# Performance work log

Measured on AMD Instinct MI355X. Metric: run time of the kernel, lower is better.

The kernel has to match this reference:

```python
import jax, jax.numpy as jnp
import numpy as np

B, S, H, NH, HD = 2, 2048, 4096, 32, 128
NEG = jnp.finfo(jnp.float32).min


def rotate_half(x):
    x1, x2 = x[..., : x.shape[-1] // 2], x[..., x.shape[-1] // 2 :]
    return jnp.concatenate((-x2, x1), axis=-1)


def setup_inputs() -> dict:
    key = jax.random.key(0)
    ks = jax.random.split(key, 7)
    return {
        "hidden_states": jax.random.normal(ks[0], (B, S, H), jnp.float32),
        "cos": jax.random.uniform(ks[1], (1, 1, S, HD), jnp.float32),
        "sin": jax.random.uniform(ks[2], (1, 1, S, HD), jnp.float32),
        "Wq": jax.random.normal(ks[3], (H, H), jnp.float32) * 0.02,
        "Wk": jax.random.normal(ks[4], (HD, H), jnp.float32) * 0.02,
        "Wv": jax.random.normal(ks[5], (HD, H), jnp.float32) * 0.02,
        "Wd": jax.random.normal(ks[6], (H, H), jnp.float32) * 0.02,
    }


def reference(hidden_states, cos, sin, Wq, Wk, Wv, Wd):
    b, s, _ = hidden_states.shape
    q = (hidden_states @ Wq.T).reshape(b, s, NH, HD).transpose(0, 2, 1, 3)  # [B,NH,S,HD]
    k = (hidden_states @ Wk.T)[:, None, :, :]  # [B,1,S,HD] (multi-query)
    v = (hidden_states @ Wv.T)[:, None, :, :]
    # inline RoPE
    q = q * cos + rotate_half(q) * sin
    k = k * cos + rotate_half(k) * sin
    scale = 1.0 / jnp.sqrt(jnp.float32(HD))
    scores = jnp.einsum("bhqd,bhkd->bhqk", q, k) * scale
    # causal mask: additive finfo.min above diagonal
    causal = jnp.tril(jnp.ones((s, s), jnp.bool_))
    scores = scores + jnp.where(causal, 0.0, NEG)
    attn = jax.nn.softmax(scores, axis=-1)
    out = jnp.einsum("bhqk,bhkd->bhqd", attn, v)  # [B,NH,S,HD]
    out = out.transpose(0, 2, 1, 3).reshape(b, s, NH * HD)
    return out @ Wd.T
```

## Files before the change

kernel.cpp:

```cpp
#include <hip/hip_runtime.h>
#include <hip/hip_bf16.h>

constexpr int Bc  = 2;
constexpr int Sc  = 2048;
constexpr int Hc  = 4096;
constexpr int NHc = 32;
constexpr int HDc = 128;

typedef __attribute__((ext_vector_type(8))) __bf16 bf16x8;
typedef __attribute__((ext_vector_type(4))) __bf16 bf16x4;
typedef __attribute__((ext_vector_type(4))) float  f32x4;

#if defined(__has_builtin)
#if __has_builtin(__builtin_amdgcn_global_load_lds)
#define HAS_GLL 1
#endif
#endif
#ifndef HAS_GLL
#define HAS_GLL 0
#endif

__device__ __forceinline__ void gll16(const __bf16* g, __bf16* lds_base, int lane) {
#if HAS_GLL
    __builtin_amdgcn_global_load_lds((const __attribute__((address_space(1))) void*)g,
                                     (__attribute__((address_space(3))) void*)lds_base,
                                     16, 0, 0);
#else
    *(int4*)(lds_base + lane * 8) = *(const int4*)g;
#endif
}

__global__ void cvt_f32_bf16(const float* __restrict__ in, __bf16* __restrict__ out, int n) {
    int i = (blockIdx.x * blockDim.x + threadIdx.x) * 4;
    if (i >= n) return;
    const float4 v = *(const float4*)(in + i);
    bf16x4 o;
    o[0] = (__bf16)v.x; o[1] = (__bf16)v.y; o[2] = (__bf16)v.z; o[3] = (__bf16)v.w;
    *(bf16x4*)(out + i) = o;
}

__global__ void build_wkv(const float* __restrict__ Wk, const float* __restrict__ Wv,
                          __bf16* __restrict__ out) {
    int i = (blockIdx.x * blockDim.x + threadIdx.x) * 4;
    if (i >= 256 * Hc) return;
    int row = i >> 12;
    int col = i & (Hc - 1);
    const float* src = (row < HDc) ? (Wk + (long)row * Hc + col)
                                   : (Wv + (long)(row - HDc) * Hc + col);
    const float4 v = *(const float4*)src;
    bf16x4 o;
    o[0] = (__bf16)v.x; o[1] = (__bf16)v.y; o[2] = (__bf16)v.z; o[3] = (__bf16)v.w;
    *(bf16x4*)(out + i) = o;
}

template <typename OUT>
__global__ __launch_bounds__(256)
void gemm_bt(const __bf16* __restrict__ A, const __bf16* __restrict__ B,
             OUT* __restrict__ C, int M, int N, int K) {
    __shared__ __bf16 As[128][64];
    __shared__ __bf16 Bs[128][64];

    const int tid  = threadIdx.x;
    const int wave = tid >> 6, lane = tid & 63;
    const int lrow = lane & 15, quad = lane >> 4;
    const int m0   = blockIdx.y * 128;
    const int n0   = blockIdx.x * 128;
    const int wr   = (wave >> 1) * 64;
    const int wc   = (wave & 1) * 64;

    f32x4 acc[4][4] = {};

    int srow[4], scol[4];
#pragma unroll
    for (int it = 0; it < 4; ++it) {
        int e = (wave * 4 + it) * 1024 + lane * 16;
        int r = e >> 7;
        int cb = (e >> 4) & 7;
        srow[it] = r;
        scol[it] = ((cb ^ (r & 7)) * 8);
    }
    const __bf16* Ab = A + (long)m0 * K;
    const __bf16* Bb = B + (long)n0 * K;

    const int fcol0 = ((quad ^ (lrow & 7)) << 3);
    const int fcol1 = (((4 | quad) ^ (lrow & 7)) << 3);

    const int nk = K >> 6;
    for (int kt = 0; kt < nk; ++kt) {
        const long k0 = (long)kt * 64;
        __syncthreads();
#pragma unroll
        for (int it = 0; it < 4; ++it)
            gll16(Ab + (long)srow[it] * K + k0 + scol[it], &As[0][0] + (wave * 4 + it) * 512, lane);
#pragma unroll
        for (int it = 0; it < 4; ++it)
            gll16(Bb + (long)srow[it] * K + k0 + scol[it], &Bs[0][0] + (wave * 4 + it) * 512, lane);
        __syncthreads();

#pragma unroll
        for (int c = 0; c < 2; ++c) {
            const int fc = c ? fcol1 : fcol0;
            bf16x8 af[4], bfv[4];
#pragma unroll
            for (int i = 0; i < 4; ++i) af[i]  = *(const bf16x8*)&As[wr + i * 16 + lrow][fc];
#pragma unroll
            for (int j = 0; j < 4; ++j) bfv[j] = *(const bf16x8*)&Bs[wc + j * 16 + lrow][fc];
#pragma unroll
            for (int i = 0; i < 4; ++i)
#pragma unroll
                for (int j = 0; j < 4; ++j)
                    acc[i][j] = __builtin_amdgcn_mfma_f32_16x16x32_bf16(af[i], bfv[j], acc[i][j], 0, 0, 0);
        }
    }

#pragma unroll
    for (int i = 0; i < 4; ++i) {
        const int row = m0 + wr + i * 16 + quad * 4;
#pragma unroll
        for (int j = 0; j < 4; ++j) {
            const int col = n0 + wc + j * 16 + lrow;
            OUT* cp = C + (long)row * N + col;
#pragma unroll
            for (int r = 0; r < 4; ++r) cp[(long)r * N] = (OUT)acc[i][j][r];
        }
    }
}

template <typename OUT>
__global__ __launch_bounds__(256)
void gemm_bt64(const __bf16* __restrict__ A, const __bf16* __restrict__ B,
               OUT* __restrict__ C, int M, int N, int K) {
    __shared__ __bf16 As[64][64];
    __shared__ __bf16 Bs[64][64];

    const int tid  = threadIdx.x;
    const int wave = tid >> 6, lane = tid & 63;
    const int lrow = lane & 15, quad = lane >> 4;
    const int m0   = blockIdx.y * 64;
    const int n0   = blockIdx.x * 64;
    const int wr   = (wave >> 1) * 32;
    const int wc   = (wave & 1) * 32;

    f32x4 acc[2][2] = {};

    int srow[2], scol[2];
#pragma unroll
    for (int it = 0; it < 2; ++it) {
        int e = (wave * 2 + it) * 1024 + lane * 16;
        int r = e >> 7;
        int cb = (e >> 4) & 7;
        srow[it] = r;
        scol[it] = ((cb ^ (r & 7)) * 8);
    }
    const __bf16* Ab = A + (long)m0 * K;
    const __bf16* Bb = B + (long)n0 * K;

    const int fcol0 = ((quad ^ (lrow & 7)) << 3);
    const int fcol1 = (((4 | quad) ^ (lrow & 7)) << 3);

    const int nk = K >> 6;
    for (int kt = 0; kt < nk; ++kt) {
        const long k0 = (long)kt * 64;
        __syncthreads();
#pragma unroll
        for (int it = 0; it < 2; ++it)
            gll16(Ab + (long)srow[it] * K + k0 + scol[it], &As[0][0] + (wave * 2 + it) * 512, lane);
#pragma unroll
        for (int it = 0; it < 2; ++it)
            gll16(Bb + (long)srow[it] * K + k0 + scol[it], &Bs[0][0] + (wave * 2 + it) * 512, lane);
        __syncthreads();

#pragma unroll
        for (int c = 0; c < 2; ++c) {
            const int fc = c ? fcol1 : fcol0;
            bf16x8 af[2], bfv[2];
#pragma unroll
            for (int i = 0; i < 2; ++i) af[i]  = *(const bf16x8*)&As[wr + i * 16 + lrow][fc];
#pragma unroll
            for (int j = 0; j < 2; ++j) bfv[j] = *(const bf16x8*)&Bs[wc + j * 16 + lrow][fc];
#pragma unroll
            for (int i = 0; i < 2; ++i)
#pragma unroll
                for (int j = 0; j < 2; ++j)
                    acc[i][j] = __builtin_amdgcn_mfma_f32_16x16x32_bf16(af[i], bfv[j], acc[i][j], 0, 0, 0);
        }
    }

#pragma unroll
    for (int i = 0; i < 2; ++i) {
        const int row = m0 + wr + i * 16 + quad * 4;
#pragma unroll
        for (int j = 0; j < 2; ++j) {
            const int col = n0 + wc + j * 16 + lrow;
            OUT* cp = C + (long)row * N + col;
#pragma unroll
            for (int r = 0; r < 4; ++r) cp[(long)r * N] = (OUT)acc[i][j][r];
        }
    }
}

__global__ void rope_q(__bf16* __restrict__ Q, const float* __restrict__ cosb,
                       const float* __restrict__ sinb, float scale) {
    int gid  = blockIdx.x * blockDim.x + threadIdx.x;
    int row  = gid >> 8;
    int rem  = gid & 255;
    int h    = rem >> 3;
    int dblk = (rem & 7) * 8;
    int s    = row & (Sc - 1);
    __bf16* p = Q + (long)row * Hc + h * HDc;
    const float* cp = cosb + s * HDc;
    const float* sp = sinb + s * HDc;
    bf16x8 lo = *(bf16x8*)(p + dblk);
    bf16x8 hi = *(bf16x8*)(p + dblk + 64);
    bf16x8 olo, ohi;
#pragma unroll
    for (int j = 0; j < 8; ++j) {
        float ql = (float)lo[j], qh = (float)hi[j];
        float cl = cp[dblk + j],      sl = sp[dblk + j];
        float ch = cp[dblk + 64 + j], sh = sp[dblk + 64 + j];
        olo[j] = (__bf16)((ql * cl - qh * sl) * scale);
        ohi[j] = (__bf16)((qh * ch + ql * sh) * scale);
    }
    *(bf16x8*)(p + dblk)      = olo;
    *(bf16x8*)(p + dblk + 64) = ohi;
}

__global__ void rope_k(__bf16* __restrict__ KV, const float* __restrict__ cosb,
                       const float* __restrict__ sinb) {
    int gid  = blockIdx.x * blockDim.x + threadIdx.x;
    int row  = gid >> 3;
    int dblk = (gid & 7) * 8;
    int s    = row & (Sc - 1);
    __bf16* p = KV + (long)row * 256;
    const float* cp = cosb + s * HDc;
    const float* sp = sinb + s * HDc;
    bf16x8 lo = *(bf16x8*)(p + dblk);
    bf16x8 hi = *(bf16x8*)(p + dblk + 64);
    bf16x8 olo, ohi;
#pragma unroll
    for (int j = 0; j < 8; ++j) {
        float ql = (float)lo[j], qh = (float)hi[j];
        float cl = cp[dblk + j],      sl = sp[dblk + j];
        float ch = cp[dblk + 64 + j], sh = sp[dblk + 64 + j];
        olo[j] = (__bf16)(ql * cl - qh * sl);
        ohi[j] = (__bf16)(qh * ch + ql * sh);
    }
    *(bf16x8*)(p + dblk)      = olo;
    *(bf16x8*)(p + dblk + 64) = ohi;
}

__global__ void vtrans(const __bf16* __restrict__ KV, __bf16* __restrict__ Vt) {
    __shared__ __bf16 T[128][72];
    const int tid = threadIdx.x;
    const int s0  = (blockIdx.x & (Sc / 64 - 1)) * 64;
    const int b   = blockIdx.x / (Sc / 64);
#pragma unroll
    for (int i = 0; i < 4; ++i) {
        int e = i * 256 + tid;
        int s = e >> 4, dc = (e & 15) * 8;
        bf16x8 v = *(const bf16x8*)(KV + (long)(b * Sc + s0 + s) * 256 + 128 + dc);
#pragma unroll
        for (int j = 0; j < 8; ++j) T[dc + j][s] = v[j];
    }
    __syncthreads();
#pragma unroll
    for (int i = 0; i < 4; ++i) {
        int e = i * 256 + tid;
        int d = e >> 3, sc8 = (e & 7) * 8;
        bf16x8 v;
#pragma unroll
        for (int j = 0; j < 8; ++j) v[j] = T[d][sc8 + j];
        *(bf16x8*)(Vt + (long)(b * HDc + d) * Sc + s0 + sc8) = v;
    }
}

__global__ __launch_bounds__(256, 2)
void attn(const __bf16* __restrict__ Q,
          const __bf16* __restrict__ KV,
          const __bf16* __restrict__ Vt,
          __bf16* __restrict__ O) {
    const int qt   = (gridDim.x - 1) - blockIdx.x;
    const int bh   = blockIdx.y;
    const int b    = bh >> 5, h = bh & 31;
    const int tid  = threadIdx.x;
    const int wave = tid >> 6, lane = tid & 63;
    const int lrow = lane & 15, quad = lane >> 4;

    __shared__ __bf16 Ks[2][64][128];
    __shared__ __bf16 Vs[2][128][64];
    __shared__ __bf16 Vones[16][72];
    __shared__ __bf16 Ps[4][16][72];

    for (int idx = tid; idx < 16 * 72; idx += 256)
        Vones[idx / 72][idx % 72] = (__bf16)1.0f;

    const int q0 = qt * 128 + wave * 32;

    bf16x8 aq[2][4];
#pragma unroll
    for (int qq = 0; qq < 2; ++qq) {
        const __bf16* qp = Q + (long)(b * Sc + q0 + qq * 16 + lrow) * Hc + h * HDc + quad * 8;
#pragma unroll
        for (int c = 0; c < 4; ++c) aq[qq][c] = *(const bf16x8*)(qp + c * 32);
    }

    f32x4 o[2][8] = {};
    f32x4 lac[2] = {};
    float mst[2][4];
#pragma unroll
    for (int qq = 0; qq < 2; ++qq)
#pragma unroll
        for (int r = 0; r < 4; ++r) mst[qq][r] = -3.0e38f;

    const __bf16* kvb = KV + (long)b * Sc * 256;
    const __bf16* vtb = Vt + (long)b * HDc * Sc;
    int krow[4], kcol[4], vrow[4], vcol[4];
#pragma unroll
    for (int it = 0; it < 4; ++it) {
        int e = (wave * 4 + it) * 1024 + lane * 16;
        int rk = e >> 8, cbk = (e >> 4) & 15;
        krow[it] = rk; kcol[it] = ((cbk ^ (rk & 15)) * 8);
        int rv = e >> 7, cbv = (e >> 4) & 7;
        vrow[it] = rv; vcol[it] = ((cbv ^ (rv & 7)) * 8);
    }

    auto stage = [&](int kt, int bu) {
#pragma unroll
        for (int it = 0; it < 4; ++it) {
            gll16(kvb + (long)(kt * 64 + krow[it]) * 256 + kcol[it],
                  &Ks[bu][0][0] + (wave * 4 + it) * 512, lane);
            gll16(vtb + (long)vrow[it] * Sc + kt * 64 + vcol[it],
                  &Vs[bu][0][0] + (wave * 4 + it) * 512, lane);
        }
    };

    const int nt = 2 * qt + 2;
    stage(0, 0);

    for (int kt = 0; kt < nt; ++kt) {
        __syncthreads();
        if (kt + 1 < nt) stage(kt + 1, (kt + 1) & 1);
        const int bu = kt & 1;

        f32x4 sc[2][4] = {};
#pragma unroll
        for (int ct = 0; ct < 4; ++ct) {
#pragma unroll
            for (int c = 0; c < 4; ++c) {
                bf16x8 bk = *(const bf16x8*)&Ks[bu][ct * 16 + lrow][(((c << 2) | quad) ^ lrow) << 3];
                sc[0][ct] = __builtin_amdgcn_mfma_f32_16x16x32_bf16(aq[0][c], bk, sc[0][ct], 0, 0, 0);
                sc[1][ct] = __builtin_amdgcn_mfma_f32_16x16x32_bf16(aq[1][c], bk, sc[1][ct], 0, 0, 0);
            }
        }

        bf16x8 ap[2][2];
#pragma unroll
        for (int qq = 0; qq < 2; ++qq) {
            if (kt * 64 + 63 > q0 + qq * 16) {
#pragma unroll
                for (int ct = 0; ct < 4; ++ct) {
                    int kv = kt * 64 + ct * 16 + lrow;
#pragma unroll
                    for (int r = 0; r < 4; ++r) {
                        int qr = q0 + qq * 16 + quad * 4 + r;
                        if (kv > qr) sc[qq][ct][r] = -3.0e38f;
                    }
                }
            }

            float mnewv[4], alf[4];
#pragma unroll
            for (int r = 0; r < 4; ++r) {
                float mx = fmaxf(fmaxf(sc[qq][0][r], sc[qq][1][r]), fmaxf(sc[qq][2][r], sc[qq][3][r]));
#pragma unroll
                for (int off = 1; off < 16; off <<= 1) mx = fmaxf(mx, __shfl_xor(mx, off, 64));
                float mnew = fmaxf(mst[qq][r], mx);
                alf[r]   = __expf(mst[qq][r] - mnew);
                mst[qq][r] = mnew;
                mnewv[r] = mnew;
            }
#pragma unroll
            for (int ct = 0; ct < 4; ++ct)
#pragma unroll
                for (int r = 0; r < 4; ++r)
                    sc[qq][ct][r] = __expf(sc[qq][ct][r] - mnewv[r]);
#pragma unroll
            for (int dt = 0; dt < 8; ++dt)
#pragma unroll
                for (int r = 0; r < 4; ++r) o[qq][dt][r] *= alf[r];
#pragma unroll
            for (int r = 0; r < 4; ++r) lac[qq][r] *= alf[r];

#pragma unroll
            for (int ct = 0; ct < 4; ++ct)
#pragma unroll
                for (int r = 0; r < 4; ++r)
                    Ps[wave][quad * 4 + r][ct * 16 + lrow] = (__bf16)sc[qq][ct][r];
#pragma unroll
            for (int ks = 0; ks < 2; ++ks)
                ap[qq][ks] = *(const bf16x8*)&Ps[wave][lrow][ks * 32 + quad * 8];
        }

#pragma unroll
        for (int dt = 0; dt < 8; ++dt) {
#pragma unroll
            for (int ks = 0; ks < 2; ++ks) {
                bf16x8 bv = *(const bf16x8*)&Vs[bu][dt * 16 + lrow]
                                [(((ks << 2) | quad) ^ (lrow & 7)) << 3];
#pragma unroll
                for (int qq = 0; qq < 2; ++qq)
                    o[qq][dt] = __builtin_amdgcn_mfma_f32_16x16x32_bf16(ap[qq][ks], bv, o[qq][dt], 0, 0, 0);
            }
        }
#pragma unroll
        for (int ks = 0; ks < 2; ++ks) {
            bf16x8 bv = *(const bf16x8*)&Vones[lrow][ks * 32 + quad * 8];
#pragma unroll
            for (int qq = 0; qq < 2; ++qq)
                lac[qq] = __builtin_amdgcn_mfma_f32_16x16x32_bf16(ap[qq][ks], bv, lac[qq], 0, 0, 0);
        }
    }

#pragma unroll
    for (int qq = 0; qq < 2; ++qq)
#pragma unroll
        for (int r = 0; r < 4; ++r) {
            float inv = 1.f / lac[qq][r];
            int qr = q0 + qq * 16 + quad * 4 + r;
            __bf16* op = O + (long)(b * Sc + qr) * Hc + h * HDc;
#pragma unroll
            for (int dt = 0; dt < 8; ++dt) op[dt * 16 + lrow] = (__bf16)(o[qq][dt][r] * inv);
        }
}

extern "C" void kernel_launch(void* const* d_in, const int* in_sizes, int n_in,
                              void* d_out, int out_size, void* d_ws, size_t ws_size,
                              hipStream_t stream) {
    const float* hs   = (const float*)d_in[0];
    const float* cosb = (const float*)d_in[1];
    const float* sinb = (const float*)d_in[2];
    const float* Wq   = (const float*)d_in[3];
    const float* Wk   = (const float*)d_in[4];
    const float* Wv   = (const float*)d_in[5];
    const float* Wd   = (const float*)d_in[6];
    float* out = (float*)d_out;

    char* ws = (char*)d_ws;
    const long SZ_HS  = (long)Bc * Sc * Hc * 2;
    const long SZ_W   = (long)Hc * Hc * 2;
    const long SZ_KV  = (long)Bc * Sc * 256 * 2;
    __bf16* hs16  = (__bf16*)(ws);
    __bf16* wq16  = (__bf16*)(ws + SZ_HS);
    __bf16* wkv16 = (__bf16*)(ws + SZ_HS + SZ_W);
    __bf16* q16   = (__bf16*)(ws + SZ_HS + SZ_W + SZ_KV);
    __bf16* kv16  = (__bf16*)(ws + SZ_HS + SZ_W + SZ_KV + SZ_HS);
    __bf16* vt16  = (__bf16*)(ws + SZ_HS + SZ_W + SZ_KV + SZ_HS + SZ_KV);
    __bf16* att16 = hs16;
    __bf16* wd16  = wq16;

    const int nHS = Bc * Sc * Hc;
    const int nW  = Hc * Hc;

    cvt_f32_bf16<<<nHS / 1024, 256, 0, stream>>>(hs, hs16, nHS);
    cvt_f32_bf16<<<nW / 1024, 256, 0, stream>>>(Wq, wq16, nW);
    build_wkv<<<(256 * Hc) / 1024, 256, 0, stream>>>(Wk, Wv, wkv16);

    gemm_bt<__bf16><<<dim3(Hc / 128, (Bc * Sc) / 128), 256, 0, stream>>>(
        hs16, wq16, q16, Bc * Sc, Hc, Hc);
    gemm_bt64<__bf16><<<dim3(256 / 64, (Bc * Sc) / 64), 256, 0, stream>>>(
        hs16, wkv16, kv16, Bc * Sc, 256, Hc);

    cvt_f32_bf16<<<nW / 1024, 256, 0, stream>>>(Wd, wd16, nW);

    const float scale = 0.08838834764831845f;
    rope_q<<<(Bc * Sc * NHc * 8) / 256, 256, 0, stream>>>(q16, cosb, sinb, scale);
    rope_k<<<(Bc * Sc * 8) / 256, 256, 0, stream>>>(kv16, cosb, sinb);
    vtrans<<<Bc * (Sc / 64), 256, 0, stream>>>(kv16, vt16);

    attn<<<dim3(Sc / 128, Bc * NHc), 256, 0, stream>>>(q16, kv16, vt16, att16);

    gemm_bt<float><<<dim3(Hc / 128, (Bc * Sc) / 128), 256, 0, stream>>>(
        att16, wd16, out, Bc * Sc, Hc, Hc);
}
```

Before: 804.6 us.

## Read K/V directly from global memory in attention, drop LDS staging

Removes the double-buffered LDS staging of K and V tiles in the attention kernel. MFMA B-operands are now loaded straight from global memory (relying on L1/L2 for reuse across waves), and the per-tile __syncthreads is dropped. Less shared memory lets launch bounds rise to 3 blocks per CU, and s_setprio raises wave priority around the MFMA sections. The cost is more global and cache traffic with no explicit prefetch, so load latency is exposed unless extra occupancy hides it.

```diff
diff --git a/kernel.cpp b/kernel.cpp
--- a/kernel.cpp
+++ b/kernel.cpp
@@ -274,7 +274,7 @@
     }
 }
 
-__global__ __launch_bounds__(256, 2)
+__global__ __launch_bounds__(256, 3)
 void attn(const __bf16* __restrict__ Q,
           const __bf16* __restrict__ KV,
           const __bf16* __restrict__ Vt,
@@ -286,13 +286,12 @@
     const int wave = tid >> 6, lane = tid & 63;
     const int lrow = lane & 15, quad = lane >> 4;
 
-    __shared__ __bf16 Ks[2][64][128];
-    __shared__ __bf16 Vs[2][128][64];
     __shared__ __bf16 Vones[16][72];
     __shared__ __bf16 Ps[4][16][72];
 
     for (int idx = tid; idx < 16 * 72; idx += 256)
         Vones[idx / 72][idx % 72] = (__bf16)1.0f;
+    __syncthreads();
 
     const int q0 = qt * 128 + wave * 32;
 
@@ -314,44 +313,23 @@
 
     const __bf16* kvb = KV + (long)b * Sc * 256;
     const __bf16* vtb = Vt + (long)b * HDc * Sc;
-    int krow[4], kcol[4], vrow[4], vcol[4];
-#pragma unroll
-    for (int it = 0; it < 4; ++it) {
-        int e = (wave * 4 + it) * 1024 + lane * 16;
-        int rk = e >> 8, cbk = (e >> 4) & 15;
-        krow[it] = rk; kcol[it] = ((cbk ^ (rk & 15)) * 8);
-        int rv = e >> 7, cbv = (e >> 4) & 7;
-        vrow[it] = rv; vcol[it] = ((cbv ^ (rv & 7)) * 8);
-    }
-
-    auto stage = [&](int kt, int bu) {
-#pragma unroll
-        for (int it = 0; it < 4; ++it) {
-            gll16(kvb + (long)(kt * 64 + krow[it]) * 256 + kcol[it],
-                  &Ks[bu][0][0] + (wave * 4 + it) * 512, lane);
-            gll16(vtb + (long)vrow[it] * Sc + kt * 64 + vcol[it],
-                  &Vs[bu][0][0] + (wave * 4 + it) * 512, lane);
-        }
-    };
 
     const int nt = 2 * qt + 2;
-    stage(0, 0);
 
     for (int kt = 0; kt < nt; ++kt) {
-        __syncthreads();
-        if (kt + 1 < nt) stage(kt + 1, (kt + 1) & 1);
-        const int bu = kt & 1;
-
         f32x4 sc[2][4] = {};
+        __builtin_amdgcn_s_setprio(1);
 #pragma unroll
         for (int ct = 0; ct < 4; ++ct) {
+            const __bf16* kp = kvb + (long)(kt * 64 + ct * 16 + lrow) * 256 + quad * 8;
 #pragma unroll
             for (int c = 0; c < 4; ++c) {
-                bf16x8 bk = *(const bf16x8*)&Ks[bu][ct * 16 + lrow][(((c << 2) | quad) ^ lrow) << 3];
+                bf16x8 bk = *(const bf16x8*)(kp + c * 32);
                 sc[0][ct] = __builtin_amdgcn_mfma_f32_16x16x32_bf16(aq[0][c], bk, sc[0][ct], 0, 0, 0);
                 sc[1][ct] = __builtin_amdgcn_mfma_f32_16x16x32_bf16(aq[1][c], bk, sc[1][ct], 0, 0, 0);
             }
         }
+        __builtin_amdgcn_s_setprio(0);
 
         bf16x8 ap[2][2];
 #pragma unroll
@@ -401,12 +379,13 @@
                 ap[qq][ks] = *(const bf16x8*)&Ps[wave][lrow][ks * 32 + quad * 8];
         }
 
+        __builtin_amdgcn_s_setprio(1);
 #pragma unroll
         for (int dt = 0; dt < 8; ++dt) {
+            const __bf16* vp = vtb + (long)(dt * 16 + lrow) * Sc + kt * 64 + quad * 8;
 #pragma unroll
             for (int ks = 0; ks < 2; ++ks) {
-                bf16x8 bv = *(const bf16x8*)&Vs[bu][dt * 16 + lrow]
-                                [(((ks << 2) | quad) ^ (lrow & 7)) << 3];
+                bf16x8 bv = *(const bf16x8*)(vp + ks * 32);
 #pragma unroll
                 for (int qq = 0; qq < 2; ++qq)
                     o[qq][dt] = __builtin_amdgcn_mfma_f32_16x16x32_bf16(ap[qq][ks], bv, o[qq][dt], 0, 0, 0);
@@ -419,6 +398,7 @@
             for (int qq = 0; qq < 2; ++qq)
                 lac[qq] = __builtin_amdgcn_mfma_f32_16x16x32_bf16(ap[qq][ks], bv, lac[qq], 0, 0, 0);
         }
+        __builtin_amdgcn_s_setprio(0);
     }
 
 #pragma unroll
```

Result: slower. 1.205 ms (+49.8%).
